# Kernel optimization log

Hardware: AMD Instinct MI355X
Metric: run time of the kernel (lower is better)

Reference implementation:

```python
import jax, jax.numpy as jnp
import numpy as np

B, H, S, D = 2, 16, 2048, 64  # depth = dmodel / num_heads
DMODEL = H * D


def setup_inputs() -> dict:
    key = jax.random.key(0)
    kq, kk, kv, kw = jax.random.split(key, 4)
    Q = jax.random.normal(kq, (B, H, S, D), dtype=jnp.float32)
    K = jax.random.normal(kk, (B, H, S, D), dtype=jnp.float32)
    V = jax.random.normal(kv, (B, H, S, D), dtype=jnp.float32)
    W = jax.random.normal(kw, (DMODEL, DMODEL), dtype=jnp.float32) * (1.0 / np.sqrt(DMODEL))
    b = jnp.zeros((DMODEL,), dtype=jnp.float32)
    return {"Q": Q, "K": K, "V": V, "W": W, "b": b}


def reference(Q, K, V, W, b):
    depth = Q.shape[-1]
    # scores: (B, H, S, S) -- full score matrix, matching the original math
    scores = jnp.einsum('bhqd,bhkd->bhqk', Q, K) / jnp.sqrt(jnp.float32(depth))
    attn = jax.nn.softmax(scores, axis=-1)
    vals = jnp.einsum('bhqk,bhkd->bhqd', attn, V)          # (B, H, S, D)
    vals = jnp.transpose(vals, (0, 2, 1, 3))               # (B, S, H, D)
    concat = vals.reshape(vals.shape[0], vals.shape[1], -1)  # (B, S, dmodel)
    return concat @ W + b
```

## Files before the change

### kernel.cpp

```cpp
#include <hip/hip_runtime.h>
#include <hip/hip_bf16.h>


typedef float  f32x16 __attribute__((ext_vector_type(16)));
typedef float  f32x4v __attribute__((ext_vector_type(4)));
typedef __bf16 bf16x8 __attribute__((ext_vector_type(8)));
typedef __bf16 bf16x4 __attribute__((ext_vector_type(4)));

static constexpr int Bn = 2, Hn = 16, Sn = 2048, Dn = 64, DM = 1024;
static constexpr size_t QKV_ELEMS = (size_t)Bn * Hn * Sn * Dn;

#define QSCALE 0.18033688011112042f

static __device__ __forceinline__ unsigned pack2(float a, float b) {
  union { __bf16 h; unsigned short s; } ua, ub;
  ua.h = (__bf16)a; ub.h = (__bf16)b;
  return (unsigned)ua.s | ((unsigned)ub.s << 16);
}

__global__ __launch_bounds__(256) void convert_qk(
    const float* __restrict__ q, const float* __restrict__ k,
    __bf16* __restrict__ qo, __bf16* __restrict__ ko) {
  const int z = blockIdx.y;
  const float* src = z ? k : q;
  __bf16* dst      = z ? ko : qo;
  const float scale = z ? 1.0f : QSCALE;
  size_t i = ((size_t)blockIdx.x * 256 + threadIdx.x) * 8;
  f32x4v a = *(const f32x4v*)(src + i);
  f32x4v b = *(const f32x4v*)(src + i + 4);
  bf16x8 o;
#pragma unroll
  for (int j = 0; j < 4; ++j) { o[j] = (__bf16)(a[j] * scale); o[4 + j] = (__bf16)(b[j] * scale); }
  *(bf16x8*)(dst + i) = o;
}

__global__ __launch_bounds__(256) void convert_vt(const float* __restrict__ v,
                                                  __bf16* __restrict__ vt) {
  __shared__ __bf16 T[64][72];
  const int t = threadIdx.x, r = t >> 2, c0 = (t & 3) * 16;
  const int kv0 = blockIdx.x * 64, bh = blockIdx.y;
  const float* src = v + ((size_t)bh * Sn + kv0 + r) * Dn + c0;
#pragma unroll
  for (int i = 0; i < 4; ++i) {
    f32x4v f = *(const f32x4v*)(src + i * 4);
#pragma unroll
    for (int j = 0; j < 4; ++j) T[r][c0 + i * 4 + j] = (__bf16)f[j];
  }
  __syncthreads();
  const int dr = t >> 2, k0 = (t & 3) * 16;
  bf16x8 o0, o1;
#pragma unroll
  for (int i = 0; i < 8; ++i) { o0[i] = T[k0 + i][dr]; o1[i] = T[k0 + 8 + i][dr]; }
  __bf16* dst = vt + ((size_t)bh * Dn + dr) * Sn + kv0 + k0;
  *(bf16x8*)dst = o0;
  *(bf16x8*)(dst + 8) = o1;
}

__global__ __launch_bounds__(256) void convert_w(const float* __restrict__ w,
                                                 __bf16* __restrict__ wt) {
  __shared__ __bf16 T[64][72];
  const int t = threadIdx.x, r = t >> 2, c0 = (t & 3) * 16;
  const int nt = blockIdx.x * 64, kt = blockIdx.y * 64;
  const float* src = w + (size_t)(kt + r) * DM + nt + c0;
#pragma unroll
  for (int i = 0; i < 4; ++i) {
    f32x4v f = *(const f32x4v*)(src + i * 4);
#pragma unroll
    for (int j = 0; j < 4; ++j) T[r][c0 + i * 4 + j] = (__bf16)f[j];
  }
  __syncthreads();
  bf16x8 o0, o1;
#pragma unroll
  for (int i = 0; i < 8; ++i) { o0[i] = T[c0 + i][r]; o1[i] = T[c0 + 8 + i][r]; }
  __bf16* dst = wt + (size_t)(nt + r) * DM + kt + c0;
  *(bf16x8*)dst = o0;
  *(bf16x8*)(dst + 8) = o1;
}

__global__ __launch_bounds__(256, 2) void attn(
    const __bf16* __restrict__ Qb, const __bf16* __restrict__ Kb,
    const __bf16* __restrict__ Vtg, __bf16* __restrict__ Cc) {
  const int tid = threadIdx.x;
  const int wave = tid >> 6, lane = tid & 63;
  const int ln = lane & 31, g = lane >> 5;
  const int qb = blockIdx.x, h = blockIdx.y, bz = blockIdx.z;

  __shared__ __bf16 Ks[2][64][72];
  __shared__ __bf16 Vs[2][64][72];

  const size_t hoff = (size_t)(bz * Hn + h) * Sn * Dn;
  const __bf16* Qp = Qb + hoff + (size_t)(qb * 128 + wave * 32) * Dn;
  const __bf16* Kp = Kb + hoff;
  const __bf16* Vp = Vtg + hoff;

  bf16x8 qf[4];
#pragma unroll
  for (int ks = 0; ks < 4; ++ks)
    qf[ks] = *(const bf16x8*)(Qp + (size_t)ln * Dn + ks * 16 + g * 8);

  const int sr = tid >> 2, sc = (tid & 3) * 16;
  bf16x8 k0r, k1r, v0r, v1r;
  {
    const __bf16* kp = Kp + (size_t)sr * Dn + sc;
    k0r = *(const bf16x8*)kp; k1r = *(const bf16x8*)(kp + 8);
    const __bf16* vp = Vp + (size_t)sr * Sn + sc;
    v0r = *(const bf16x8*)vp; v1r = *(const bf16x8*)(vp + 8);
  }

  f32x16 O0 = {}, O1 = {};
  float Lown = 0.0f;

  for (int kt = 0; kt < Sn / 64; ++kt) {
    const int buf = kt & 1;
    *(bf16x8*)&Ks[buf][sr][sc]     = k0r;
    *(bf16x8*)&Ks[buf][sr][sc + 8] = k1r;
    *(bf16x8*)&Vs[buf][sr][sc]     = v0r;
    *(bf16x8*)&Vs[buf][sr][sc + 8] = v1r;
    __syncthreads();

    if (kt < Sn / 64 - 1) {
      const __bf16* kp = Kp + (size_t)((kt + 1) * 64 + sr) * Dn + sc;
      k0r = *(const bf16x8*)kp; k1r = *(const bf16x8*)(kp + 8);
      const __bf16* vp = Vp + (size_t)sr * Sn + (kt + 1) * 64 + sc;
      v0r = *(const bf16x8*)vp; v1r = *(const bf16x8*)(vp + 8);
    }

    float p[32];
#pragma unroll
    for (int mt = 0; mt < 2; ++mt) {
      f32x16 s = {};
#pragma unroll
      for (int ks = 0; ks < 4; ++ks) {
        bf16x8 kf = *(const bf16x8*)&Ks[buf][mt * 32 + ln][ks * 16 + g * 8];
        s = __builtin_amdgcn_mfma_f32_32x32x16_bf16(kf, qf[ks], s, 0, 0, 0);
      }
#pragma unroll
      for (int r = 0; r < 16; ++r) p[mt * 16 + r] = __builtin_amdgcn_exp2f(s[r]);
    }
    float sum = 0.0f;
#pragma unroll
    for (int r = 0; r < 32; ++r) sum += p[r];
    Lown += sum;

    unsigned w[16];
#pragma unroll
    for (int t = 0; t < 8; ++t) {
      w[t]     = pack2(p[2 * t], p[2 * t + 1]);
      w[8 + t] = pack2(p[16 + 2 * t], p[16 + 2 * t + 1]);
    }

#pragma unroll
    for (int s4 = 0; s4 < 4; ++s4) {
      const int wb = (s4 >> 1) * 8 + (s4 & 1) * 4;
      unsigned xs0 = g ? w[wb + 0] : w[wb + 2];
      unsigned xs1 = g ? w[wb + 1] : w[wb + 3];
      unsigned x0 = (unsigned)__shfl_xor((int)xs0, 32);
      unsigned x1 = (unsigned)__shfl_xor((int)xs1, 32);
      union { unsigned u[4]; bf16x8 v; } pu;
      pu.u[0] = g ? x0 : w[wb + 0];
      pu.u[1] = g ? x1 : w[wb + 1];
      pu.u[2] = g ? w[wb + 2] : x0;
      pu.u[3] = g ? w[wb + 3] : x1;
      bf16x8 vf0 = *(const bf16x8*)&Vs[buf][ln][s4 * 16 + g * 8];
      bf16x8 vf1 = *(const bf16x8*)&Vs[buf][32 + ln][s4 * 16 + g * 8];
      O0 = __builtin_amdgcn_mfma_f32_32x32x16_bf16(vf0, pu.v, O0, 0, 0, 0);
      O1 = __builtin_amdgcn_mfma_f32_32x32x16_bf16(vf1, pu.v, O1, 0, 0, 0);
    }
    __syncthreads();
  }

  const float Lfull = Lown + __shfl_xor(Lown, 32);
  const float inv = 1.0f / Lfull;
  __bf16* Osb = ((__bf16*)Ks) + wave * 32 * 72;
#pragma unroll
  for (int mtD = 0; mtD < 2; ++mtD) {
#pragma unroll
    for (int a = 0; a < 4; ++a) {
      const f32x16 O = mtD ? O1 : O0;
      bf16x4 t4;
#pragma unroll
      for (int c = 0; c < 4; ++c) t4[c] = (__bf16)(O[4 * a + c] * inv);
      *(bf16x4*)(Osb + ln * 72 + mtD * 32 + 8 * a + 4 * g) = t4;
    }
  }
  const int q0w = qb * 128 + wave * 32;
#pragma unroll
  for (int i = 0; i < 4; ++i) {
    const int rq = i * 8 + (lane >> 3);
    const int c8 = (lane & 7) * 8;
    bf16x8 o = *(const bf16x8*)(Osb + rq * 72 + c8);
    size_t base = (((size_t)bz * Sn + q0w + rq) * Hn + h) * Dn + c8;
    *(bf16x8*)&Cc[base] = o;
  }
}

__global__ __launch_bounds__(256, 2) void proj(
    const __bf16* __restrict__ A, const __bf16* __restrict__ Wt,
    const float* __restrict__ bias, float* __restrict__ out) {
  const int tid = threadIdx.x, wave = tid >> 6, lane = tid & 63;
  const int ln = lane & 31, g = lane >> 5;
  const int bm = blockIdx.x, bn = blockIdx.y;
  __shared__ __bf16 As[2][128][72];
  __shared__ __bf16 Bs[2][64][72];
  const int ar = tid >> 1, ac = (tid & 1) * 32;
  const int br = tid >> 2, bc = (tid & 3) * 16;
  f32x16 acc0 = {}, acc1 = {};
  const __bf16* Ap = A + (size_t)(bm * 128) * DM;
  const __bf16* Wp = Wt + (size_t)(bn * 64) * DM;

  bf16x8 a0, a1, a2, a3, b0, b1;
  {
    const __bf16* ap = Ap + (size_t)ar * DM + ac;
    a0 = *(const bf16x8*)ap;        a1 = *(const bf16x8*)(ap + 8);
    a2 = *(const bf16x8*)(ap + 16); a3 = *(const bf16x8*)(ap + 24);
    const __bf16* wp = Wp + (size_t)br * DM + bc;
    b0 = *(const bf16x8*)wp; b1 = *(const bf16x8*)(wp + 8);
  }

  for (int kt = 0; kt < DM / 64; ++kt) {
    const int buf = kt & 1;
    *(bf16x8*)&As[buf][ar][ac]      = a0;
    *(bf16x8*)&As[buf][ar][ac + 8]  = a1;
    *(bf16x8*)&As[buf][ar][ac + 16] = a2;
    *(bf16x8*)&As[buf][ar][ac + 24] = a3;
    *(bf16x8*)&Bs[buf][br][bc]      = b0;
    *(bf16x8*)&Bs[buf][br][bc + 8]  = b1;
    __syncthreads();
    if (kt < DM / 64 - 1) {
      const __bf16* ap = Ap + (size_t)ar * DM + (kt + 1) * 64 + ac;
      a0 = *(const bf16x8*)ap;        a1 = *(const bf16x8*)(ap + 8);
      a2 = *(const bf16x8*)(ap + 16); a3 = *(const bf16x8*)(ap + 24);
      const __bf16* wp = Wp + (size_t)br * DM + (kt + 1) * 64 + bc;
      b0 = *(const bf16x8*)wp; b1 = *(const bf16x8*)(wp + 8);
    }
#pragma unroll
    for (int ks = 0; ks < 4; ++ks) {
      bf16x8 af  = *(const bf16x8*)&As[buf][wave * 32 + ln][ks * 16 + g * 8];
      bf16x8 wf0 = *(const bf16x8*)&Bs[buf][ln][ks * 16 + g * 8];
      bf16x8 wf1 = *(const bf16x8*)&Bs[buf][32 + ln][ks * 16 + g * 8];
      acc0 = __builtin_amdgcn_mfma_f32_32x32x16_bf16(af, wf0, acc0, 0, 0, 0);
      acc1 = __builtin_amdgcn_mfma_f32_32x32x16_bf16(af, wf1, acc1, 0, 0, 0);
    }
    __syncthreads();
  }
  float bv0 = bias[bn * 64 + ln], bv1 = bias[bn * 64 + 32 + ln];
#pragma unroll
  for (int r = 0; r < 16; ++r) {
    int row = bm * 128 + wave * 32 + (r & 3) + ((r >> 2) << 3) + (g << 2);
    out[(size_t)row * DM + bn * 64 + ln]      = acc0[r] + bv0;
    out[(size_t)row * DM + bn * 64 + 32 + ln] = acc1[r] + bv1;
  }
}

extern "C" void kernel_launch(void* const* d_in, const int* in_sizes, int n_in,
                              void* d_out, int out_size, void* d_ws, size_t ws_size,
                              hipStream_t stream) {
  const float* Q = (const float*)d_in[0];
  const float* K = (const float*)d_in[1];
  const float* V = (const float*)d_in[2];
  const float* W = (const float*)d_in[3];
  const float* b = (const float*)d_in[4];
  float* out = (float*)d_out;

  __bf16* ws  = (__bf16*)d_ws;
  __bf16* Qb  = ws;
  __bf16* Kb  = Qb + QKV_ELEMS;
  __bf16* Vtg = Kb + QKV_ELEMS;
  __bf16* Cc  = Vtg + QKV_ELEMS;
  __bf16* Wt  = Cc + QKV_ELEMS;

  convert_qk<<<dim3((unsigned)(QKV_ELEMS / (256 * 8)), 2, 1), 256, 0, stream>>>(Q, K, Qb, Kb);
  convert_vt<<<dim3(Sn / 64, Bn * Hn, 1), 256, 0, stream>>>(V, Vtg);
  convert_w<<<dim3(DM / 64, DM / 64, 1), 256, 0, stream>>>(W, Wt);
  attn<<<dim3(Sn / 128, Hn, Bn), 256, 0, stream>>>(Qb, Kb, Vtg, Cc);
  proj<<<dim3(Bn * Sn / 128, DM / 64, 1), 256, 0, stream>>>(Cc, Wt, b, out);
}
```

Measured before the change: 167.8 us.

## Restage attention and GEMM pipelines, packed bf16 converts, paired LDS transposes

After: 163.6 us. -2.6%, faster.

```diff
diff --git a/kernel.cpp b/kernel.cpp
--- a/kernel.cpp
+++ b/kernel.cpp
@@ -4,18 +4,38 @@
 
 typedef float  f32x16 __attribute__((ext_vector_type(16)));
 typedef float  f32x4v __attribute__((ext_vector_type(4)));
+typedef float  f32x2v __attribute__((ext_vector_type(2)));
 typedef __bf16 bf16x8 __attribute__((ext_vector_type(8)));
 typedef __bf16 bf16x4 __attribute__((ext_vector_type(4)));
+typedef __bf16 bf16x2 __attribute__((ext_vector_type(2)));
 
 static constexpr int Bn = 2, Hn = 16, Sn = 2048, Dn = 64, DM = 1024;
 static constexpr size_t QKV_ELEMS = (size_t)Bn * Hn * Sn * Dn;
 
 #define QSCALE 0.18033688011112042f
 
+#if __has_builtin(__builtin_amdgcn_cvt_pk_bf16_f32)
+static __device__ __forceinline__ unsigned pack2(float a, float b) {
+  bf16x2 t = __builtin_amdgcn_cvt_pk_bf16_f32(a, b);
+  union { bf16x2 v; unsigned u; } c; c.v = t; return c.u;
+}
+#else
 static __device__ __forceinline__ unsigned pack2(float a, float b) {
   union { __bf16 h; unsigned short s; } ua, ub;
   ua.h = (__bf16)a; ub.h = (__bf16)b;
   return (unsigned)ua.s | ((unsigned)ub.s << 16);
+}
+#endif
+
+static __device__ __forceinline__ void unzip8(const unsigned* wds, bf16x8* r0, bf16x8* r1) {
+  union { unsigned u[4]; bf16x8 v; } a, b;
+#pragma unroll
+  for (int i = 0; i < 4; ++i) {
+    unsigned lo = wds[2 * i], hi = wds[2 * i + 1];
+    a.u[i] = (lo & 0xffffu) | (hi << 16);
+    b.u[i] = (lo >> 16) | (hi & 0xffff0000u);
+  }
+  *r0 = a.v; *r1 = b.v;
 }
 
 __global__ __launch_bounds__(256) void convert_qk(
@@ -36,48 +56,75 @@
 
 __global__ __launch_bounds__(256) void convert_vt(const float* __restrict__ v,
                                                   __bf16* __restrict__ vt) {
-  __shared__ __bf16 T[64][72];
+  __shared__ __bf16 T[64][74];
   const int t = threadIdx.x, r = t >> 2, c0 = (t & 3) * 16;
   const int kv0 = blockIdx.x * 64, bh = blockIdx.y;
   const float* src = v + ((size_t)bh * Sn + kv0 + r) * Dn + c0;
-#pragma unroll
-  for (int i = 0; i < 4; ++i) {
+  union { bf16x8 v8; unsigned u[4]; } o0, o1;
+#pragma unroll
+  for (int i = 0; i < 2; ++i) {
     f32x4v f = *(const f32x4v*)(src + i * 4);
 #pragma unroll
-    for (int j = 0; j < 4; ++j) T[r][c0 + i * 4 + j] = (__bf16)f[j];
+    for (int j = 0; j < 4; ++j) o0.v8[i * 4 + j] = (__bf16)f[j];
+  }
+#pragma unroll
+  for (int i = 0; i < 2; ++i) {
+    f32x4v f = *(const f32x4v*)(src + 8 + i * 4);
+#pragma unroll
+    for (int j = 0; j < 4; ++j) o1.v8[i * 4 + j] = (__bf16)f[j];
+  }
+#pragma unroll
+  for (int j = 0; j < 4; ++j) {
+    *(unsigned*)&T[r][c0 + 2 * j]     = o0.u[j];
+    *(unsigned*)&T[r][c0 + 8 + 2 * j] = o1.u[j];
   }
   __syncthreads();
-  const int dr = t >> 2, k0 = (t & 3) * 16;
-  bf16x8 o0, o1;
-#pragma unroll
-  for (int i = 0; i < 8; ++i) { o0[i] = T[k0 + i][dr]; o1[i] = T[k0 + 8 + i][dr]; }
-  __bf16* dst = vt + ((size_t)bh * Dn + dr) * Sn + kv0 + k0;
-  *(bf16x8*)dst = o0;
-  *(bf16x8*)(dst + 8) = o1;
+  const int rp = t >> 3, k0 = (t & 7) * 8;
+  unsigned wds[8];
+#pragma unroll
+  for (int i = 0; i < 8; ++i) wds[i] = *(const unsigned*)&T[k0 + i][2 * rp];
+  bf16x8 r0, r1; unzip8(wds, &r0, &r1);
+  __bf16* dst = vt + ((size_t)bh * Dn + 2 * rp) * Sn + kv0 + k0;
+  *(bf16x8*)dst = r0;
+  *(bf16x8*)(dst + Sn) = r1;
 }
 
 __global__ __launch_bounds__(256) void convert_w(const float* __restrict__ w,
                                                  __bf16* __restrict__ wt) {
-  __shared__ __bf16 T[64][72];
+  __shared__ __bf16 T[64][74];
   const int t = threadIdx.x, r = t >> 2, c0 = (t & 3) * 16;
   const int nt = blockIdx.x * 64, kt = blockIdx.y * 64;
   const float* src = w + (size_t)(kt + r) * DM + nt + c0;
-#pragma unroll
-  for (int i = 0; i < 4; ++i) {
+  union { bf16x8 v8; unsigned u[4]; } o0, o1;
+#pragma unroll
+  for (int i = 0; i < 2; ++i) {
     f32x4v f = *(const f32x4v*)(src + i * 4);
 #pragma unroll
-    for (int j = 0; j < 4; ++j) T[r][c0 + i * 4 + j] = (__bf16)f[j];
+    for (int j = 0; j < 4; ++j) o0.v8[i * 4 + j] = (__bf16)f[j];
+  }
+#pragma unroll
+  for (int i = 0; i < 2; ++i) {
+    f32x4v f = *(const f32x4v*)(src + 8 + i * 4);
+#pragma unroll
+    for (int j = 0; j < 4; ++j) o1.v8[i * 4 + j] = (__bf16)f[j];
+  }
+#pragma unroll
+  for (int j = 0; j < 4; ++j) {
+    *(unsigned*)&T[r][c0 + 2 * j]     = o0.u[j];
+    *(unsigned*)&T[r][c0 + 8 + 2 * j] = o1.u[j];
   }
   __syncthreads();
-  bf16x8 o0, o1;
-#pragma unroll
-  for (int i = 0; i < 8; ++i) { o0[i] = T[c0 + i][r]; o1[i] = T[c0 + 8 + i][r]; }
-  __bf16* dst = wt + (size_t)(nt + r) * DM + kt + c0;
-  *(bf16x8*)dst = o0;
-  *(bf16x8*)(dst + 8) = o1;
-}
-
-__global__ __launch_bounds__(256, 2) void attn(
+  const int rp = t >> 3, k0 = (t & 7) * 8;
+  unsigned wds[8];
+#pragma unroll
+  for (int i = 0; i < 8; ++i) wds[i] = *(const unsigned*)&T[k0 + i][2 * rp];
+  bf16x8 r0, r1; unzip8(wds, &r0, &r1);
+  __bf16* dst = wt + (size_t)(nt + 2 * rp) * DM + kt + k0;
+  *(bf16x8*)dst = r0;
+  *(bf16x8*)(dst + DM) = r1;
+}
+
+__global__ __launch_bounds__(256, 4) void attn(
     const __bf16* __restrict__ Qb, const __bf16* __restrict__ Kb,
     const __bf16* __restrict__ Vtg, __bf16* __restrict__ Cc) {
   const int tid = threadIdx.x;
@@ -99,31 +146,27 @@
     qf[ks] = *(const bf16x8*)(Qp + (size_t)ln * Dn + ks * 16 + g * 8);
 
   const int sr = tid >> 2, sc = (tid & 3) * 16;
-  bf16x8 k0r, k1r, v0r, v1r;
-  {
-    const __bf16* kp = Kp + (size_t)sr * Dn + sc;
-    k0r = *(const bf16x8*)kp; k1r = *(const bf16x8*)(kp + 8);
-    const __bf16* vp = Vp + (size_t)sr * Sn + sc;
-    v0r = *(const bf16x8*)vp; v1r = *(const bf16x8*)(vp + 8);
-  }
+  const __bf16* kbase = Kp + (size_t)sr * Dn + sc;
+  const __bf16* vbase = Vp + (size_t)sr * Sn + sc;
+
+  bf16x8 k0r = *(const bf16x8*)kbase, k1r = *(const bf16x8*)(kbase + 8);
+  bf16x8 v0r = *(const bf16x8*)vbase, v1r = *(const bf16x8*)(vbase + 8);
+  *(bf16x8*)&Ks[0][sr][sc]     = k0r;
+  *(bf16x8*)&Ks[0][sr][sc + 8] = k1r;
+  *(bf16x8*)&Vs[0][sr][sc]     = v0r;
+  *(bf16x8*)&Vs[0][sr][sc + 8] = v1r;
+  k0r = *(const bf16x8*)(kbase + (size_t)64 * Dn);
+  k1r = *(const bf16x8*)(kbase + (size_t)64 * Dn + 8);
+  v0r = *(const bf16x8*)(vbase + 64);
+  v1r = *(const bf16x8*)(vbase + 64 + 8);
+  __syncthreads();
 
   f32x16 O0 = {}, O1 = {};
   float Lown = 0.0f;
-
-  for (int kt = 0; kt < Sn / 64; ++kt) {
+  constexpr int NT = Sn / 64;
+
+  for (int kt = 0; kt < NT; ++kt) {
     const int buf = kt & 1;
-    *(bf16x8*)&Ks[buf][sr][sc]     = k0r;
-    *(bf16x8*)&Ks[buf][sr][sc + 8] = k1r;
-    *(bf16x8*)&Vs[buf][sr][sc]     = v0r;
-    *(bf16x8*)&Vs[buf][sr][sc + 8] = v1r;
-    __syncthreads();
-
-    if (kt < Sn / 64 - 1) {
-      const __bf16* kp = Kp + (size_t)((kt + 1) * 64 + sr) * Dn + sc;
-      k0r = *(const bf16x8*)kp; k1r = *(const bf16x8*)(kp + 8);
-      const __bf16* vp = Vp + (size_t)sr * Sn + (kt + 1) * 64 + sc;
-      v0r = *(const bf16x8*)vp; v1r = *(const bf16x8*)(vp + 8);
-    }
 
     float p[32];
 #pragma unroll
@@ -137,16 +180,33 @@
 #pragma unroll
       for (int r = 0; r < 16; ++r) p[mt * 16 + r] = __builtin_amdgcn_exp2f(s[r]);
     }
-    float sum = 0.0f;
-#pragma unroll
-    for (int r = 0; r < 32; ++r) sum += p[r];
-    Lown += sum;
+    f32x2v s2 = {0.0f, 0.0f};
+#pragma unroll
+    for (int tt = 0; tt < 16; ++tt) {
+      f32x2v t2 = {p[2 * tt], p[2 * tt + 1]};
+      s2 += t2;
+    }
+    Lown += s2[0] + s2[1];
 
     unsigned w[16];
 #pragma unroll
-    for (int t = 0; t < 8; ++t) {
-      w[t]     = pack2(p[2 * t], p[2 * t + 1]);
-      w[8 + t] = pack2(p[16 + 2 * t], p[16 + 2 * t + 1]);
+    for (int tt = 0; tt < 8; ++tt) {
+      w[tt]     = pack2(p[2 * tt], p[2 * tt + 1]);
+      w[8 + tt] = pack2(p[16 + 2 * tt], p[16 + 2 * tt + 1]);
+    }
+
+    if (kt + 1 < NT) {
+      const int nb = buf ^ 1;
+      *(bf16x8*)&Ks[nb][sr][sc]     = k0r;
+      *(bf16x8*)&Ks[nb][sr][sc + 8] = k1r;
+      *(bf16x8*)&Vs[nb][sr][sc]     = v0r;
+      *(bf16x8*)&Vs[nb][sr][sc + 8] = v1r;
+      if (kt + 2 < NT) {
+        const __bf16* kp = kbase + (size_t)(kt + 2) * 64 * Dn;
+        k0r = *(const bf16x8*)kp; k1r = *(const bf16x8*)(kp + 8);
+        const __bf16* vp = vbase + (kt + 2) * 64;
+        v0r = *(const bf16x8*)vp; v1r = *(const bf16x8*)(vp + 8);
+      }
     }
 
 #pragma unroll
@@ -216,23 +276,24 @@
     const __bf16* wp = Wp + (size_t)br * DM + bc;
     b0 = *(const bf16x8*)wp; b1 = *(const bf16x8*)(wp + 8);
   }
-
-  for (int kt = 0; kt < DM / 64; ++kt) {
+  *(bf16x8*)&As[0][ar][ac]      = a0;
+  *(bf16x8*)&As[0][ar][ac + 8]  = a1;
+  *(bf16x8*)&As[0][ar][ac + 16] = a2;
+  *(bf16x8*)&As[0][ar][ac + 24] = a3;
+  *(bf16x8*)&Bs[0][br][bc]      = b0;
+  *(bf16x8*)&Bs[0][br][bc + 8]  = b1;
+  {
+    const __bf16* ap = Ap + (size_t)ar * DM + 64 + ac;
+    a0 = *(const bf16x8*)ap;        a1 = *(const bf16x8*)(ap + 8);
+    a2 = *(const bf16x8*)(ap + 16); a3 = *(const bf16x8*)(ap + 24);
+    const __bf16* wp = Wp + (size_t)br * DM + 64 + bc;
+    b0 = *(const bf16x8*)wp; b1 = *(const bf16x8*)(wp + 8);
+  }
+  __syncthreads();
+
+  constexpr int KT = DM / 64;
+  for (int kt = 0; kt < KT; ++kt) {
     const int buf = kt & 1;
-    *(bf16x8*)&As[buf][ar][ac]      = a0;
-    *(bf16x8*)&As[buf][ar][ac + 8]  = a1;
-    *(bf16x8*)&As[buf][ar][ac + 16] = a2;
-    *(bf16x8*)&As[buf][ar][ac + 24] = a3;
-    *(bf16x8*)&Bs[buf][br][bc]      = b0;
-    *(bf16x8*)&Bs[buf][br][bc + 8]  = b1;
-    __syncthreads();
-    if (kt < DM / 64 - 1) {
-      const __bf16* ap = Ap + (size_t)ar * DM + (kt + 1) * 64 + ac;
-      a0 = *(const bf16x8*)ap;        a1 = *(const bf16x8*)(ap + 8);
-      a2 = *(const bf16x8*)(ap + 16); a3 = *(const bf16x8*)(ap + 24);
-      const __bf16* wp = Wp + (size_t)br * DM + (kt + 1) * 64 + bc;
-      b0 = *(const bf16x8*)wp; b1 = *(const bf16x8*)(wp + 8);
-    }
 #pragma unroll
     for (int ks = 0; ks < 4; ++ks) {
       bf16x8 af  = *(const bf16x8*)&As[buf][wave * 32 + ln][ks * 16 + g * 8];
@@ -240,6 +301,22 @@
       bf16x8 wf1 = *(const bf16x8*)&Bs[buf][32 + ln][ks * 16 + g * 8];
       acc0 = __builtin_amdgcn_mfma_f32_32x32x16_bf16(af, wf0, acc0, 0, 0, 0);
       acc1 = __builtin_amdgcn_mfma_f32_32x32x16_bf16(af, wf1, acc1, 0, 0, 0);
+    }
+    if (kt + 1 < KT) {
+      const int nb = buf ^ 1;
+      *(bf16x8*)&As[nb][ar][ac]      = a0;
+      *(bf16x8*)&As[nb][ar][ac + 8]  = a1;
+      *(bf16x8*)&As[nb][ar][ac + 16] = a2;
+      *(bf16x8*)&As[nb][ar][ac + 24] = a3;
+      *(bf16x8*)&Bs[nb][br][bc]      = b0;
+      *(bf16x8*)&Bs[nb][br][bc + 8]  = b1;
+      if (kt + 2 < KT) {
+        const __bf16* ap = Ap + (size_t)ar * DM + (kt + 2) * 64 + ac;
+        a0 = *(const bf16x8*)ap;        a1 = *(const bf16x8*)(ap + 8);
+        a2 = *(const bf16x8*)(ap + 16); a3 = *(const bf16x8*)(ap + 24);
+        const __bf16* wp = Wp + (size_t)br * DM + (kt + 2) * 64 + bc;
+        b0 = *(const bf16x8*)wp; b1 = *(const bf16x8*)(wp + 8);
+      }
     }
     __syncthreads();
   }
```
